# Kernel optimization log

Measured on AMD Instinct MI355X. Metric: run time of the kernel, lower is better.

Reference implementation:

```python
import jax, jax.numpy as jnp
import numpy as np
import math

N_HEAD = 16

def _c(a):
    # stack real/imag -> complex64
    return jax.lax.complex(a[..., 0], a[..., 1])

def _rope_phasor(T, D, dtype=jnp.float32):
    inv_freq = 1.0 / (10000.0 ** (jnp.arange(D, dtype=dtype) / D))
    t = jnp.arange(T, dtype=dtype)
    freqs = jnp.outer(t, inv_freq)  # [T, D]
    return jax.lax.complex(jnp.cos(freqs), jnp.sin(freqs))

def setup_inputs() -> dict:
    key = jax.random.key(0)
    ks = jax.random.split(key, 9)
    B, T, C = 2, 1024, 1024
    s = 0.02
    return {
        "x":  jax.random.normal(ks[0], (B, T, C, 2), jnp.float32),
        "wq": jax.random.normal(ks[1], (C, C, 2), jnp.float32) * s,
        "bq": jax.random.normal(ks[2], (C, 2), jnp.float32) * s,
        "wk": jax.random.normal(ks[3], (C, C, 2), jnp.float32) * s,
        "bk": jax.random.normal(ks[4], (C, 2), jnp.float32) * s,
        "wv": jax.random.normal(ks[5], (C, C, 2), jnp.float32) * s,
        "bv": jax.random.normal(ks[6], (C, 2), jnp.float32) * s,
        "wo": jax.random.normal(ks[7], (C, C, 2), jnp.float32) * s,
        "bo": jax.random.normal(ks[8], (C, 2), jnp.float32) * s,
    }

def reference(x, wq, bq, wk, bk, wv, bv, wo, bo):
    B, T, C, _ = x.shape
    H = N_HEAD
    D = C // H
    xc = _c(x)
    # complex linear projections: y = x @ W^T + b
    q = xc @ _c(wq).T + _c(bq)
    k = xc @ _c(wk).T + _c(bk)
    v = xc @ _c(wv).T + _c(bv)
    # [B, T, C] -> [B, H, T, D]
    q = q.reshape(B, T, H, D).transpose(0, 2, 1, 3)
    k = k.reshape(B, T, H, D).transpose(0, 2, 1, 3)
    v = v.reshape(B, T, H, D).transpose(0, 2, 1, 3)
    # complex RoPE phasor multiply
    ph = _rope_phasor(T, D)[None, None]  # [1,1,T,D]
    q = q * ph
    k = k * ph
    # complex QK^H, scaled
    score = jnp.einsum('bhtd,bhsd->bhts', q, jnp.conj(k)) / math.sqrt(D)
    # softmax over magnitude, then real-valued complex weights
    attn = jax.nn.softmax(jnp.abs(score), axis=-1)
    attn_c = jax.lax.complex(attn, jnp.zeros_like(attn))
    out = jnp.einsum('bhts,bhsd->bhtd', attn_c, v)
    out = out.transpose(0, 2, 1, 3).reshape(B, T, C)
    out = out @ _c(wo).T + _c(bo)
    # return real/imag stacked for a real-valued harness
    return jnp.stack([out.real, out.imag], axis=-1)
```

## Files before the change

kernel.cpp:

```cpp
#include <hip/hip_runtime.h>
#include <math.h>

#define T_SEQ  1024
#define C_DIM  1024
#define NH_    16
#define H_DIM  64
#define SCL    (0.125f * 1.4426950408889634f)

typedef __bf16 bf16;
typedef __bf16 bf16x4 __attribute__((ext_vector_type(4)));
typedef __bf16 bf16x8 __attribute__((ext_vector_type(8)));
typedef float  f32x4  __attribute__((ext_vector_type(4)));

template<bool B> struct BC { static constexpr bool value = B; };

#define MFMA16(a, b, c) __builtin_amdgcn_mfma_f32_16x16x32_bf16(a, b, c, 0, 0, 0)

#define GLOAD_LDS16(g, l) __builtin_amdgcn_global_load_lds( \
    (const __attribute__((address_space(1))) void*)(g),     \
    (__attribute__((address_space(3))) void*)(l), 16, 0, 0)

__device__ __forceinline__ bf16x8 neg8(bf16x8 x) {
    union { bf16x8 v; unsigned int u[4]; } t;
    t.v = x;
    t.u[0] ^= 0x80008000u; t.u[1] ^= 0x80008000u;
    t.u[2] ^= 0x80008000u; t.u[3] ^= 0x80008000u;
    return t.v;
}

__device__ __forceinline__ bf16x8 frag_sw(const bf16* plane, int row, int chunk) {
    int c = chunk ^ (row & 7);
    return *(const bf16x8*)&plane[row * 64 + c * 8];
}
__device__ __forceinline__ bf16x8 frag_sw4(const bf16* plane, int row, int chunk) {
    int c = chunk ^ (row & 3);
    return *(const bf16x8*)&plane[row * 32 + c * 8];
}
__device__ __forceinline__ bf16x8 frag_sw4b(const bf16* plane, int row, int chunk) {
    int c = chunk ^ ((row >> 1) & 3);
    return *(const bf16x8*)&plane[row * 32 + c * 8];
}

__global__ __launch_bounds__(256)
void split_all(const float* __restrict__ x,  const float* __restrict__ wq,
               const float* __restrict__ wk, const float* __restrict__ wv,
               const float* __restrict__ wo,
               bf16* Xr, bf16* Xi, bf16* Wqr, bf16* Wqi, bf16* Wkr, bf16* Wki,
               bf16* Wvr, bf16* Wvi, bf16* Wor, bf16* Woi,
               float* __restrict__ rope)
{
    int z = blockIdx.y;
    if (z == 5) {
        if (blockIdx.x >= 256) return;
        int idx = blockIdx.x * 256 + threadIdx.x;
        int tp = idx >> 6, d = idx & 63;
        float invf = exp2f((float)d * -0.2076205059304601f);
        float fr = (float)tp * invf;
        float sn, cs; sincosf(fr, &sn, &cs);
        *(float2*)&rope[(size_t)idx * 2] = make_float2(cs, sn);
        return;
    }
    if (z > 0 && blockIdx.x >= 512) return;
    const float* in; bf16 *pr, *pi;
    if      (z == 0) { in = x;  pr = Xr;  pi = Xi;  }
    else if (z == 1) { in = wq; pr = Wqr; pi = Wqi; }
    else if (z == 2) { in = wk; pr = Wkr; pi = Wki; }
    else if (z == 3) { in = wv; pr = Wvr; pi = Wvi; }
    else             { in = wo; pr = Wor; pi = Woi; }
    int idx = (blockIdx.x * 256 + threadIdx.x) * 8;
    bf16x8 r, im;
#pragma unroll
    for (int j = 0; j < 4; j++) {
        float4 v = *(const float4*)(in + (size_t)idx * 2 + j * 4);
        r[2*j]   = (bf16)v.x; im[2*j]   = (bf16)v.y;
        r[2*j+1] = (bf16)v.z; im[2*j+1] = (bf16)v.w;
    }
    *(bf16x8*)(pr + idx) = r;
    *(bf16x8*)(pi + idx) = im;
}

__global__ __launch_bounds__(512, 2)
void qkv_gemm(const bf16* __restrict__ Xr, const bf16* __restrict__ Xi,
              const bf16* __restrict__ Wqr, const bf16* __restrict__ Wqi,
              const bf16* __restrict__ Wkr, const bf16* __restrict__ Wki,
              const bf16* __restrict__ Wvr, const bf16* __restrict__ Wvi,
              const float* __restrict__ bq, const float* __restrict__ bk,
              const float* __restrict__ bv, const float* __restrict__ rope,
              bf16* Qr, bf16* Qi, bf16* Kr, bf16* Ki, bf16* Vr, bf16* Vi)
{
    __shared__ __attribute__((aligned(16))) bf16 smem[61440];
    const int t = threadIdx.x, lane = t & 63, wave = t >> 6;
    const int wm = (wave >> 1) * 32, wn = (wave & 1) * 32;
    const int lm = lane & 15, quad = lane >> 4;
    const int lr4 = lane >> 2, sc4q = ((lane & 3) ^ ((lane >> 3) & 3)) * 8;
    const int h = blockIdx.x, m0 = blockIdx.y * 128, n0 = h * 64;

    auto stage1 = [&](bf16* bb_, int j, int k0) {
        int c = wave + 8 * j;
        const bf16* src; bf16* dst;
        if (c < 8)       {                 src = Xr  + (size_t)(m0 + c * 16 + lr4) * C_DIM + k0 + sc4q; dst = bb_ + c * 512; }
        else if (c < 16) { int u = c - 8;  src = Xi  + (size_t)(m0 + u * 16 + lr4) * C_DIM + k0 + sc4q; dst = bb_ + 4096  + u * 512; }
        else if (c < 20) { int u = c - 16; src = Wqr + (size_t)(n0 + u * 16 + lr4) * C_DIM + k0 + sc4q; dst = bb_ + 8192  + u * 512; }
        else if (c < 24) { int u = c - 20; src = Wqi + (size_t)(n0 + u * 16 + lr4) * C_DIM + k0 + sc4q; dst = bb_ + 10240 + u * 512; }
        else if (c < 28) { int u = c - 24; src = Wkr + (size_t)(n0 + u * 16 + lr4) * C_DIM + k0 + sc4q; dst = bb_ + 12288 + u * 512; }
        else if (c < 32) { int u = c - 28; src = Wki + (size_t)(n0 + u * 16 + lr4) * C_DIM + k0 + sc4q; dst = bb_ + 14336 + u * 512; }
        else if (c < 36) { int u = c - 32; src = Wvr + (size_t)(n0 + u * 16 + lr4) * C_DIM + k0 + sc4q; dst = bb_ + 16384 + u * 512; }
        else             { int u = c - 36; src = Wvi + (size_t)(n0 + u * 16 + lr4) * C_DIM + k0 + sc4q; dst = bb_ + 18432 + u * 512; }
        GLOAD_LDS16(src, dst);
    };

    f32x4 accr[3][2][2], acci[3][2][2];
#pragma unroll
    for (int p = 0; p < 3; p++)
#pragma unroll
        for (int i = 0; i < 2; i++)
#pragma unroll
            for (int j = 0; j < 2; j++) { accr[p][i][j] = (f32x4)0.f; acci[p][i][j] = (f32x4)0.f; }

    auto step = [&](auto DOSTAGE, auto DRAIN, int bufsel, int sbsel, int k2) {
        const bf16* buf = smem + bufsel * 20480;
        bf16* sb = smem + sbsel * 20480;
        if constexpr (DRAIN.value)
            asm volatile("s_waitcnt vmcnt(0)\n\ts_barrier" ::: "memory");
        else
            asm volatile("s_waitcnt vmcnt(5)\n\ts_barrier" ::: "memory");

        bf16x8 ar[2], ai_[2], br_[2], bi_[2], bn_[2];
#pragma unroll
        for (int i = 0; i < 2; i++) {
            ar[i]  = frag_sw4b(buf,        wm + i * 16 + lm, quad);
            ai_[i] = frag_sw4b(buf + 4096, wm + i * 16 + lm, quad);
        }
#pragma unroll
        for (int j = 0; j < 2; j++) {
            br_[j] = frag_sw4b(buf + 8192,  wn + j * 16 + lm, quad);
            bi_[j] = frag_sw4b(buf + 10240, wn + j * 16 + lm, quad);
        }
        if constexpr (DOSTAGE.value) { stage1(sb, 0, k2); stage1(sb, 1, k2); }
        asm volatile("s_waitcnt lgkmcnt(0)" ::: "memory");
        __builtin_amdgcn_sched_barrier(0);
        __builtin_amdgcn_s_setprio(1);
#pragma unroll
        for (int j = 0; j < 2; j++) bn_[j] = neg8(bi_[j]);
#pragma unroll
        for (int i = 0; i < 2; i++)
#pragma unroll
            for (int j = 0; j < 2; j++) {
                accr[0][i][j] = MFMA16(ar[i],  br_[j], accr[0][i][j]);
                accr[0][i][j] = MFMA16(ai_[i], bn_[j], accr[0][i][j]);
                acci[0][i][j] = MFMA16(ar[i],  bi_[j], acci[0][i][j]);
                acci[0][i][j] = MFMA16(ai_[i], br_[j], acci[0][i][j]);
            }
        __builtin_amdgcn_s_setprio(0);
        __builtin_amdgcn_s_barrier();
#pragma unroll
        for (int j = 0; j < 2; j++) {
            br_[j] = frag_sw4b(buf + 12288, wn + j * 16 + lm, quad);
            bi_[j] = frag_sw4b(buf + 14336, wn + j * 16 + lm, quad);
        }
        if constexpr (DOSTAGE.value) { stage1(sb, 2, k2); stage1(sb, 3, k2); }
        asm volatile("s_waitcnt lgkmcnt(0)" ::: "memory");
        __builtin_amdgcn_sched_barrier(0);
        __builtin_amdgcn_s_setprio(1);
#pragma unroll
        for (int j = 0; j < 2; j++) bn_[j] = neg8(bi_[j]);
#pragma unroll
        for (int i = 0; i < 2; i++)
#pragma unroll
            for (int j = 0; j < 2; j++) {
                accr[1][i][j] = MFMA16(ar[i],  br_[j], accr[1][i][j]);
                accr[1][i][j] = MFMA16(ai_[i], bn_[j], accr[1][i][j]);
                acci[1][i][j] = MFMA16(ar[i],  bi_[j], acci[1][i][j]);
                acci[1][i][j] = MFMA16(ai_[i], br_[j], acci[1][i][j]);
            }
        __builtin_amdgcn_s_setprio(0);
        __builtin_amdgcn_s_barrier();
#pragma unroll
        for (int j = 0; j < 2; j++) {
            br_[j] = frag_sw4b(buf + 16384, wn + j * 16 + lm, quad);
            bi_[j] = frag_sw4b(buf + 18432, wn + j * 16 + lm, quad);
        }
        if constexpr (DOSTAGE.value) { stage1(sb, 4, k2); }
        asm volatile("s_waitcnt lgkmcnt(0)" ::: "memory");
        __builtin_amdgcn_sched_barrier(0);
        __builtin_amdgcn_s_setprio(1);
#pragma unroll
        for (int j = 0; j < 2; j++) bn_[j] = neg8(bi_[j]);
#pragma unroll
        for (int i = 0; i < 2; i++)
#pragma unroll
            for (int j = 0; j < 2; j++) {
                accr[2][i][j] = MFMA16(ar[i],  br_[j], accr[2][i][j]);
                accr[2][i][j] = MFMA16(ai_[i], bn_[j], accr[2][i][j]);
                acci[2][i][j] = MFMA16(ar[i],  bi_[j], acci[2][i][j]);
                acci[2][i][j] = MFMA16(ai_[i], br_[j], acci[2][i][j]);
            }
        __builtin_amdgcn_s_setprio(0);
    };

#pragma unroll
    for (int j = 0; j < 5; j++) stage1(smem,         j, 0);
#pragma unroll
    for (int j = 0; j < 5; j++) stage1(smem + 20480, j, 32);

    for (int base = 0; base < 30; base += 3) {
        step(BC<true>{}, BC<false>{}, 0, 2, (base + 2) * 32);
        step(BC<true>{}, BC<false>{}, 1, 0, (base + 3) * 32);
        step(BC<true>{}, BC<false>{}, 2, 1, (base + 4) * 32);
    }
    step(BC<false>{}, BC<false>{}, 0, 0, 0);
    step(BC<false>{}, BC<true >{}, 1, 0, 0);

    const int bb = m0 >> 10, tbase = m0 & (T_SEQ - 1);

#pragma unroll
    for (int p = 0; p < 2; p++) {
        const float* bias = p ? bk : bq;
#pragma unroll
        for (int i = 0; i < 2; i++)
#pragma unroll
            for (int j = 0; j < 2; j++) {
                int d = wn + j * 16 + lm;
                float2 bvv = *(const float2*)&bias[2 * (n0 + d)];
#pragma unroll
                for (int r = 0; r < 4; r++) {
                    int tpos = tbase + wm + i * 16 + quad * 4 + r;
                    float2 ph = *(const float2*)&rope[((size_t)tpos * H_DIM + d) * 2];
                    float yr = accr[p][i][j][r] + bvv.x;
                    float yi = acci[p][i][j][r] + bvv.y;
                    accr[p][i][j][r] = yr * ph.x - yi * ph.y;
                    acci[p][i][j][r] = yr * ph.y + yi * ph.x;
                }
            }
        bf16* dr = (p ? Kr : Qr) + ((size_t)(bb * NH_ + h) * T_SEQ + tbase) * H_DIM;
        bf16* di = (p ? Ki : Qi) + ((size_t)(bb * NH_ + h) * T_SEQ + tbase) * H_DIM;
#pragma unroll
        for (int pass = 0; pass < 2; pass++) {
            __syncthreads();
#pragma unroll
            for (int i = 0; i < 2; i++)
#pragma unroll
                for (int j = 0; j < 2; j++)
#pragma unroll
                    for (int r = 0; r < 4; r++)
                        smem[(wm + i * 16 + quad * 4 + r) * 72 + wn + j * 16 + lm] =
                            (bf16)(pass ? acci[p][i][j][r] : accr[p][i][j][r]);
            __syncthreads();
            bf16* dst = pass ? di : dr;
#pragma unroll
            for (int pp = 0; pp < 2; pp++) {
                int ch = t + 512 * pp;
                int row = ch >> 3, o = (ch & 7) * 8;
                *(bf16x8*)&dst[row * H_DIM + o] = *(const bf16x8*)&smem[row * 72 + o];
            }
        }
    }

    {
#pragma unroll
        for (int pass = 0; pass < 2; pass++) {
            __syncthreads();
#pragma unroll
            for (int i = 0; i < 2; i++)
#pragma unroll
                for (int j = 0; j < 2; j++) {
                    int d = wn + j * 16 + lm;
                    float2 bvv = *(const float2*)&bv[2 * (n0 + d)];
                    float bb2 = pass ? bvv.y : bvv.x;
                    bf16x4 pk;
#pragma unroll
                    for (int r = 0; r < 4; r++)
                        pk[r] = (bf16)((pass ? acci[2][i][j][r] : accr[2][i][j][r]) + bb2);
                    *(bf16x4*)&smem[d * 136 + wm + i * 16 + quad * 4] = pk;
                }
            __syncthreads();
            bf16* dst = (pass ? Vi : Vr) + ((size_t)(bb * NH_ + h) * H_DIM) * T_SEQ + tbase;
#pragma unroll
            for (int pp = 0; pp < 2; pp++) {
                int ch = t + 512 * pp;
                int row = ch >> 4, o = (ch & 15) * 8;
                *(bf16x8*)&dst[(size_t)row * T_SEQ + o] = *(const bf16x8*)&smem[row * 136 + o];
            }
        }
    }
}

__global__ __launch_bounds__(256, 4)
void out_gemm(const bf16* __restrict__ Ar, const bf16* __restrict__ Ai,
              const bf16* __restrict__ Br, const bf16* __restrict__ Bi,
              const float* __restrict__ bias, float* __restrict__ Y)
{
    __shared__ __attribute__((aligned(16))) bf16 sm[16384];
    const int t = threadIdx.x, lane = t & 63, wave = t >> 6;
    const int lm = lane & 15, quad = lane >> 4;
    const int s_lr = lane >> 3, s_c = (lane & 7) ^ s_lr;
    const int wm = (wave >> 1) * 32, wn = (wave & 1) * 32;
    const int m0 = blockIdx.y * 64, n0 = blockIdx.x * 64;

    f32x4 accr[2][2], acci[2][2];
#pragma unroll
    for (int i = 0; i < 2; i++)
#pragma unroll
        for (int j = 0; j < 2; j++) { accr[i][j] = (f32x4)0.f; acci[i][j] = (f32x4)0.f; }

    for (int k0 = 0; k0 < C_DIM; k0 += 64) {
#pragma unroll
        for (int j = 0; j < 8; j++) {
            int c = wave + 4 * j;
            const bf16* src; bf16* dst;
            if (c < 8)       {             src = Ar + (size_t)(m0 + c * 8 + s_lr) * C_DIM + k0 + s_c * 8; dst = sm + c * 512; }
            else if (c < 16) { int u = c - 8;  src = Ai + (size_t)(m0 + u * 8 + s_lr) * C_DIM + k0 + s_c * 8; dst = sm + 4096 + u * 512; }
            else if (c < 24) { int u = c - 16; src = Br + (size_t)(n0 + u * 8 + s_lr) * C_DIM + k0 + s_c * 8; dst = sm + 8192 + u * 512; }
            else             { int u = c - 24; src = Bi + (size_t)(n0 + u * 8 + s_lr) * C_DIM + k0 + s_c * 8; dst = sm + 12288 + u * 512; }
            GLOAD_LDS16(src, dst);
        }
        __syncthreads();
#pragma unroll
        for (int kh = 0; kh < 2; kh++) {
            bf16x8 ar[2], ai_[2], br_[2], bi_[2], bn_[2];
#pragma unroll
            for (int i = 0; i < 2; i++) {
                ar[i]  = frag_sw(sm,        wm + i * 16 + lm, kh * 4 + quad);
                ai_[i] = frag_sw(sm + 4096, wm + i * 16 + lm, kh * 4 + quad);
            }
#pragma unroll
            for (int j = 0; j < 2; j++) {
                br_[j] = frag_sw(sm + 8192,  wn + j * 16 + lm, kh * 4 + quad);
                bi_[j] = frag_sw(sm + 12288, wn + j * 16 + lm, kh * 4 + quad);
                bn_[j] = neg8(bi_[j]);
            }
#pragma unroll
            for (int i = 0; i < 2; i++)
#pragma unroll
                for (int j = 0; j < 2; j++) {
                    accr[i][j] = MFMA16(ar[i],  br_[j], accr[i][j]);
                    accr[i][j] = MFMA16(ai_[i], bn_[j], accr[i][j]);
                    acci[i][j] = MFMA16(ar[i],  bi_[j], acci[i][j]);
                    acci[i][j] = MFMA16(ai_[i], br_[j], acci[i][j]);
                }
        }
        __syncthreads();
    }
#pragma unroll
    for (int i = 0; i < 2; i++)
#pragma unroll
        for (int j = 0; j < 2; j++) {
            int n = n0 + wn + j * 16 + lm;
            float2 bvv = *(const float2*)&bias[2 * n];
#pragma unroll
            for (int r = 0; r < 4; r++) {
                int m = m0 + wm + i * 16 + quad * 4 + r;
                *(float2*)&Y[((size_t)m * C_DIM + n) * 2] =
                    make_float2(accr[i][j][r] + bvv.x, acci[i][j][r] + bvv.y);
            }
        }
}

__global__ __launch_bounds__(512, 4)
void attn_mfma(const bf16* __restrict__ Qpr, const bf16* __restrict__ Qpi,
               const bf16* __restrict__ Kpr, const bf16* __restrict__ Kpi,
               const bf16* __restrict__ Vtr, const bf16* __restrict__ Vti,
               bf16* __restrict__ ABr, bf16* __restrict__ ABi)
{
    __shared__ __attribute__((aligned(16))) bf16 smem[32768];
    const int t = threadIdx.x, lane = t & 63, w = t >> 6;
    const int qg = w & 3, sh = w >> 2;
    const int lm = lane & 15, quad = lane >> 4;
    const int h = blockIdx.x;
    const int q0 = blockIdx.y * 64;
    const int b = blockIdx.z;
    const size_t hb = (size_t)(b * NH_ + h) * T_SEQ * H_DIM;
    const int s_lr = lane >> 3, s_c = (lane & 7) ^ s_lr;
    const int lr4 = lane >> 2, sc4a = ((lane & 3) ^ (lr4 & 3)) * 8;

    {
        const bf16* gq = (sh ? Qpi : Qpr) + hb + (size_t)q0 * H_DIM;
        bf16* lq = smem + 16384 + sh * 4096;
#pragma unroll
        for (int j = 0; j < 2; j++) {
            int cc = qg * 2 + j;
            GLOAD_LDS16(gq + (cc * 8 + s_lr) * H_DIM + s_c * 8, lq + cc * 512);
        }
    }
    __syncthreads();

    bf16x8 qfr[2], qfi[2], nqfr[2];
#pragma unroll
    for (int kh = 0; kh < 2; kh++) {
        qfr[kh]  = frag_sw(smem + 16384, qg * 16 + lm, kh * 4 + quad);
        qfi[kh]  = frag_sw(smem + 20480, qg * 16 + lm, kh * 4 + quad);
        nqfr[kh] = neg8(qfr[kh]);
    }

#pragma unroll
    for (int pre = 0; pre < 1; pre++) {
        const int S = sh * 512;
        bf16* bd = smem + sh * 8192;
        if (qg < 2) {
            const bf16* g = (qg ? Kpi : Kpr) + hb + (size_t)S * H_DIM;
            bf16* d = bd + (qg ? 2048 : 0);
#pragma unroll
            for (int cc = 0; cc < 4; cc++)
                GLOAD_LDS16(g + (cc * 8 + s_lr) * H_DIM + s_c * 8, d + cc * 512);
        } else {
            const bf16* g = (qg == 2 ? Vtr : Vti) + hb + S;
            bf16* d = bd + (qg == 2 ? 4096 : 6144);
#pragma unroll
            for (int cc = 0; cc < 4; cc++)
                GLOAD_LDS16(g + (size_t)(cc * 16 + lr4) * T_SEQ + sc4a, d + cc * 512);
        }
    }

    f32x4 Or[4], Oi[4];
#pragma unroll
    for (int nt = 0; nt < 4; nt++) { Or[nt] = (f32x4)0.f; Oi[nt] = (f32x4)0.f; }
    float lsum = 0.f;
    const int idxA = (((2 * quad) & 3) * 16 + lm) * 4;
    const int idxB = idxA + 64;
    const bool hisel = quad >= 2;

    for (int it = 0; it < 16; it++) {
        __syncthreads();
        if (it < 15) {
            const int S = (it + 1) * 32 + sh * 512;
            bf16* bd = smem + ((it + 1) & 1) * 16384 + sh * 8192;
            if (qg < 2) {
                const bf16* g = (qg ? Kpi : Kpr) + hb + (size_t)S * H_DIM;
                bf16* d = bd + (qg ? 2048 : 0);
#pragma unroll
                for (int cc = 0; cc < 4; cc++)
                    GLOAD_LDS16(g + (cc * 8 + s_lr) * H_DIM + s_c * 8, d + cc * 512);
            } else {
                const bf16* g = (qg == 2 ? Vtr : Vti) + hb + S;
                bf16* d = bd + (qg == 2 ? 4096 : 6144);
#pragma unroll
                for (int cc = 0; cc < 4; cc++)
                    GLOAD_LDS16(g + (size_t)(cc * 16 + lr4) * T_SEQ + sc4a, d + cc * 512);
            }
        }
        const bf16* buf = smem + (it & 1) * 16384 + sh * 8192;

        union { unsigned int u[2]; bf16 b[4]; } pk[2];
        float lsA = 0.f, lsB = 0.f;
#pragma unroll
        for (int ct = 0; ct < 2; ct++) {
            f32x4 sre = (f32x4)0.f, sim = (f32x4)0.f;
            __builtin_amdgcn_s_setprio(1);
#pragma unroll
            for (int kh = 0; kh < 2; kh++) {
                bf16x8 kr = frag_sw(buf,        ct * 16 + lm, kh * 4 + quad);
                bf16x8 ki = frag_sw(buf + 2048, ct * 16 + lm, kh * 4 + quad);
                sre = MFMA16(kr, qfr[kh],  sre);
                sre = MFMA16(ki, qfi[kh],  sre);
                sim = MFMA16(kr, qfi[kh],  sim);
                sim = MFMA16(ki, nqfr[kh], sim);
            }
            __builtin_amdgcn_s_setprio(0);
#pragma unroll
            for (int r = 0; r < 4; r++) {
                float mag2 = fmaf(sre[r], sre[r], sim[r] * sim[r]);
                float p = __builtin_amdgcn_exp2f(__builtin_amdgcn_sqrtf(mag2) * SCL);
                if (ct) lsB += p; else lsA += p;
                pk[ct].b[r] = (bf16)p;
            }
        }
        lsum += lsA + lsB;

        union { unsigned int u[4]; bf16x8 v; } pf;
        {
            int a0 = __builtin_amdgcn_ds_bpermute(idxA, (int)pk[0].u[0]);
            int a1 = __builtin_amdgcn_ds_bpermute(idxA, (int)pk[1].u[0]);
            int b0 = __builtin_amdgcn_ds_bpermute(idxA, (int)pk[0].u[1]);
            int b1 = __builtin_amdgcn_ds_bpermute(idxA, (int)pk[1].u[1]);
            int c0 = __builtin_amdgcn_ds_bpermute(idxB, (int)pk[0].u[0]);
            int c1 = __builtin_amdgcn_ds_bpermute(idxB, (int)pk[1].u[0]);
            int d0 = __builtin_amdgcn_ds_bpermute(idxB, (int)pk[0].u[1]);
            int d1 = __builtin_amdgcn_ds_bpermute(idxB, (int)pk[1].u[1]);
            pf.u[0] = (unsigned int)(hisel ? a1 : a0);
            pf.u[1] = (unsigned int)(hisel ? b1 : b0);
            pf.u[2] = (unsigned int)(hisel ? c1 : c0);
            pf.u[3] = (unsigned int)(hisel ? d1 : d0);
        }

        __builtin_amdgcn_s_setprio(1);
#pragma unroll
        for (int nt = 0; nt < 4; nt++) {
            Or[nt] = MFMA16(pf.v, frag_sw4(buf + 4096, nt * 16 + lm, quad), Or[nt]);
            Oi[nt] = MFMA16(pf.v, frag_sw4(buf + 6144, nt * 16 + lm, quad), Oi[nt]);
        }
        __builtin_amdgcn_s_setprio(0);
    }

    lsum += __shfl_xor(lsum, 16);
    lsum += __shfl_xor(lsum, 32);

    __syncthreads();
    float* Of  = (float*)smem;
    float* lsc = Of + 128 * 66;
    if (sh == 1) {
#pragma unroll
        for (int nt = 0; nt < 4; nt++)
#pragma unroll
            for (int r = 0; r < 4; r++) {
                Of[((qg * 2 + 0) * 16 + quad * 4 + r) * 66 + nt * 16 + lm] = Or[nt][r];
                Of[((qg * 2 + 1) * 16 + quad * 4 + r) * 66 + nt * 16 + lm] = Oi[nt][r];
            }
        if (quad == 0) lsc[qg * 16 + lm] = lsum;
    }
    __syncthreads();
    if (sh == 0) {
        float ltot = lsum + lsc[qg * 16 + lm];
        float lv = 1.f / ltot;
        float linv[4];
#pragma unroll
        for (int r = 0; r < 4; r++)
            linv[r] = __shfl(lv, (quad << 4) + quad * 4 + r, 64);
        size_t mbase = (size_t)(b * T_SEQ + q0 + qg * 16 + quad * 4) * C_DIM;
        int colb = h * H_DIM + lm;
#pragma unroll
        for (int nt = 0; nt < 4; nt++)
#pragma unroll
            for (int r = 0; r < 4; r++) {
                float orv = Or[nt][r] + Of[((qg * 2 + 0) * 16 + quad * 4 + r) * 66 + nt * 16 + lm];
                float oiv = Oi[nt][r] + Of[((qg * 2 + 1) * 16 + quad * 4 + r) * 66 + nt * 16 + lm];
                size_t o = mbase + (size_t)r * C_DIM + colb + nt * 16;
                ABr[o] = (bf16)(orv * linv[r]);
                ABi[o] = (bf16)(oiv * linv[r]);
            }
    }
}

extern "C" void kernel_launch(void* const* d_in, const int* in_sizes, int n_in,
                              void* d_out, int out_size, void* d_ws, size_t ws_size,
                              hipStream_t stream) {
    const float* x  = (const float*)d_in[0];
    const float* wq = (const float*)d_in[1];
    const float* bq = (const float*)d_in[2];
    const float* wk = (const float*)d_in[3];
    const float* bk = (const float*)d_in[4];
    const float* wv = (const float*)d_in[5];
    const float* bv = (const float*)d_in[6];
    const float* wo = (const float*)d_in[7];
    const float* bo = (const float*)d_in[8];

    float* rope = (float*)d_ws;
    bf16* w = (bf16*)(rope + 131072);
    const size_t MSZ = (size_t)2048 * 1024;
    const size_t WSZ = (size_t)1024 * 1024;
    const size_t PSZ = (size_t)2 * NH_ * T_SEQ * H_DIM;

    bf16 *Xr = w, *Xi = Xr + MSZ;
    bf16 *Wqr = Xi + MSZ,  *Wqi = Wqr + WSZ;
    bf16 *Wkr = Wqi + WSZ, *Wki = Wkr + WSZ;
    bf16 *Wvr = Wki + WSZ, *Wvi = Wvr + WSZ;
    bf16 *Wor = Wvi + WSZ, *Woi = Wor + WSZ;
    bf16 *Qr = Woi + WSZ, *Qi = Qr + PSZ;
    bf16 *Kr = Qi + PSZ,  *Ki = Kr + PSZ;
    bf16 *Vr = Ki + PSZ,  *Vi = Vr + PSZ;
    bf16 *ABr = Vi + PSZ, *ABi = ABr + MSZ;

    split_all<<<dim3(1024, 6), 256, 0, stream>>>(x, wq, wk, wv, wo,
        Xr, Xi, Wqr, Wqi, Wkr, Wki, Wvr, Wvi, Wor, Woi, rope);

    qkv_gemm<<<dim3(16, 16), 512, 0, stream>>>(
        Xr, Xi, Wqr, Wqi, Wkr, Wki, Wvr, Wvi, bq, bk, bv, rope,
        Qr, Qi, Kr, Ki, Vr, Vi);

    attn_mfma<<<dim3(16, 16, 2), 512, 0, stream>>>(
        Qr, Qi, Kr, Ki, Vr, Vi, ABr, ABi);

    out_gemm<<<dim3(16, 32), 256, 0, stream>>>(ABr, ABi, Wor, Woi, bo, (float*)d_out);
}
```

Measured before the change: 204.9 us.

## Load K and V fragments directly from global memory in attention loop

Removes the double-buffered LDS staging of K and V tiles, along with the per-iteration block barrier, from the attention kernel. Each lane now reads its K and V MFMA fragments straight from global memory via vector loads. This drops the LDS traffic and synchronisation, but every wave re-reads the same K/V data from global memory or cache with no prefetch overlap, so load latency sits directly in front of the MFMAs.

```diff
diff --git a/kernel.cpp b/kernel.cpp
--- a/kernel.cpp
+++ b/kernel.cpp
@@ -31,10 +31,6 @@
 __device__ __forceinline__ bf16x8 frag_sw(const bf16* plane, int row, int chunk) {
     int c = chunk ^ (row & 7);
     return *(const bf16x8*)&plane[row * 64 + c * 8];
-}
-__device__ __forceinline__ bf16x8 frag_sw4(const bf16* plane, int row, int chunk) {
-    int c = chunk ^ (row & 3);
-    return *(const bf16x8*)&plane[row * 32 + c * 8];
 }
 __device__ __forceinline__ bf16x8 frag_sw4b(const bf16* plane, int row, int chunk) {
     int c = chunk ^ ((row >> 1) & 3);
@@ -371,7 +367,6 @@
     const int b = blockIdx.z;
     const size_t hb = (size_t)(b * NH_ + h) * T_SEQ * H_DIM;
     const int s_lr = lane >> 3, s_c = (lane & 7) ^ s_lr;
-    const int lr4 = lane >> 2, sc4a = ((lane & 3) ^ (lr4 & 3)) * 8;
 
     {
         const bf16* gq = (sh ? Qpi : Qpr) + hb + (size_t)q0 * H_DIM;
@@ -392,24 +387,10 @@
         nqfr[kh] = neg8(qfr[kh]);
     }
 
-#pragma unroll
-    for (int pre = 0; pre < 1; pre++) {
-        const int S = sh * 512;
-        bf16* bd = smem + sh * 8192;
-        if (qg < 2) {
-            const bf16* g = (qg ? Kpi : Kpr) + hb + (size_t)S * H_DIM;
-            bf16* d = bd + (qg ? 2048 : 0);
-#pragma unroll
-            for (int cc = 0; cc < 4; cc++)
-                GLOAD_LDS16(g + (cc * 8 + s_lr) * H_DIM + s_c * 8, d + cc * 512);
-        } else {
-            const bf16* g = (qg == 2 ? Vtr : Vti) + hb + S;
-            bf16* d = bd + (qg == 2 ? 4096 : 6144);
-#pragma unroll
-            for (int cc = 0; cc < 4; cc++)
-                GLOAD_LDS16(g + (size_t)(cc * 16 + lr4) * T_SEQ + sc4a, d + cc * 512);
-        }
-    }
+    const bf16* Kr_ = Kpr + hb;
+    const bf16* Ki_ = Kpi + hb;
+    const bf16* Vr_ = Vtr + hb;
+    const bf16* Vi_ = Vti + hb;
 
     f32x4 Or[4], Oi[4];
 #pragma unroll
@@ -418,38 +399,23 @@
     const int idxA = (((2 * quad) & 3) * 16 + lm) * 4;
     const int idxB = idxA + 64;
     const bool hisel = quad >= 2;
+    const int kcol = quad * 8;
+    const int vcol = quad * 8;
 
     for (int it = 0; it < 16; it++) {
-        __syncthreads();
-        if (it < 15) {
-            const int S = (it + 1) * 32 + sh * 512;
-            bf16* bd = smem + ((it + 1) & 1) * 16384 + sh * 8192;
-            if (qg < 2) {
-                const bf16* g = (qg ? Kpi : Kpr) + hb + (size_t)S * H_DIM;
-                bf16* d = bd + (qg ? 2048 : 0);
-#pragma unroll
-                for (int cc = 0; cc < 4; cc++)
-                    GLOAD_LDS16(g + (cc * 8 + s_lr) * H_DIM + s_c * 8, d + cc * 512);
-            } else {
-                const bf16* g = (qg == 2 ? Vtr : Vti) + hb + S;
-                bf16* d = bd + (qg == 2 ? 4096 : 6144);
-#pragma unroll
-                for (int cc = 0; cc < 4; cc++)
-                    GLOAD_LDS16(g + (size_t)(cc * 16 + lr4) * T_SEQ + sc4a, d + cc * 512);
-            }
-        }
-        const bf16* buf = smem + (it & 1) * 16384 + sh * 8192;
+        const int S = it * 32 + sh * 512;
 
         union { unsigned int u[2]; bf16 b[4]; } pk[2];
         float lsA = 0.f, lsB = 0.f;
 #pragma unroll
         for (int ct = 0; ct < 2; ct++) {
             f32x4 sre = (f32x4)0.f, sim = (f32x4)0.f;
+            const size_t krow = (size_t)(S + ct * 16 + lm) * H_DIM;
             __builtin_amdgcn_s_setprio(1);
 #pragma unroll
             for (int kh = 0; kh < 2; kh++) {
-                bf16x8 kr = frag_sw(buf,        ct * 16 + lm, kh * 4 + quad);
-                bf16x8 ki = frag_sw(buf + 2048, ct * 16 + lm, kh * 4 + quad);
+                bf16x8 kr = *(const bf16x8*)&Kr_[krow + kh * 32 + kcol];
+                bf16x8 ki = *(const bf16x8*)&Ki_[krow + kh * 32 + kcol];
                 sre = MFMA16(kr, qfr[kh],  sre);
                 sre = MFMA16(ki, qfi[kh],  sre);
                 sim = MFMA16(kr, qfi[kh],  sim);
@@ -485,8 +451,11 @@
         __builtin_amdgcn_s_setprio(1);
 #pragma unroll
         for (int nt = 0; nt < 4; nt++) {
-            Or[nt] = MFMA16(pf.v, frag_sw4(buf + 4096, nt * 16 + lm, quad), Or[nt]);
-            Oi[nt] = MFMA16(pf.v, frag_sw4(buf + 6144, nt * 16 + lm, quad), Oi[nt]);
+            const size_t vrow = (size_t)(nt * 16 + lm) * T_SEQ + S + vcol;
+            bf16x8 vr = *(const bf16x8*)&Vr_[vrow];
+            bf16x8 vi = *(const bf16x8*)&Vi_[vrow];
+            Or[nt] = MFMA16(pf.v, vr, Or[nt]);
+            Oi[nt] = MFMA16(pf.v, vi, Oi[nt]);
         }
         __builtin_amdgcn_s_setprio(0);
     }
```

Result: slower. 288.3 us (+40.7%).
